# Performance work log

Measured on AMD Instinct MI355X. Metric: run time of the kernel, lower is better.

The kernel has to match this reference:

```python
import jax, jax.numpy as jnp
import numpy as np

NEG_SLOPE = 0.2
EPS = 1e-16


def gat_conv(x, edge_index, W, att_src, att_dst, bias, heads, out_ch, concat):
    """PyG-style GATConv (eval mode, add_self_loops=True)."""
    N = x.shape[0]
    h = (x @ W).reshape(N, heads, out_ch)              # [N,H,C]
    loop = jnp.arange(N, dtype=edge_index.dtype)
    src = jnp.concatenate([edge_index[0], loop])       # [E+N]
    dst = jnp.concatenate([edge_index[1], loop])
    a_src = jnp.sum(h * att_src, axis=-1)              # [N,H]
    a_dst = jnp.sum(h * att_dst, axis=-1)
    e = jax.nn.leaky_relu(a_src[src] + a_dst[dst], NEG_SLOPE)  # [E+N,H]
    # segment softmax over destination nodes
    m = jax.ops.segment_max(e, dst, num_segments=N)
    e = jnp.exp(e - m[dst])
    s = jax.ops.segment_sum(e, dst, num_segments=N)
    alpha = e / (s[dst] + EPS)                         # [E+N,H]
    msg = h[src] * alpha[..., None]                    # [E+N,H,C]
    out = jax.ops.segment_sum(msg, dst, num_segments=N)  # [N,H,C]
    out = out.reshape(N, heads * out_ch) if concat else out.mean(axis=1)
    return out + bias


def setup_inputs() -> dict:
    key = jax.random.key(0)
    ks = jax.random.split(key, 11)
    N, F, E = 100000, 128, 1600000
    H1, C1 = 4, 16
    H2, C2 = 1, 16
    return {
        "x": jax.random.normal(ks[0], (N, F), dtype=jnp.float32),
        "edge_index": jax.random.randint(ks[1], (2, E), 0, N, dtype=jnp.int64) if jax.config.jax_enable_x64 else jax.random.randint(ks[1], (2, E), 0, N).astype(jnp.int32),
        "W1": jax.random.normal(ks[2], (F, H1 * C1), dtype=jnp.float32) * 0.1,
        "att_src1": jax.random.normal(ks[3], (H1, C1), dtype=jnp.float32) * 0.1,
        "att_dst1": jax.random.normal(ks[4], (H1, C1), dtype=jnp.float32) * 0.1,
        "bias1": jax.random.normal(ks[5], (H1 * C1,), dtype=jnp.float32) * 0.1,
        "W2": jax.random.normal(ks[6], (H1 * C1, H2 * C2), dtype=jnp.float32) * 0.1,
        "att_src2": jax.random.normal(ks[7], (H2, C2), dtype=jnp.float32) * 0.1,
        "att_dst2": jax.random.normal(ks[8], (H2, C2), dtype=jnp.float32) * 0.1,
        "bias2": jax.random.normal(ks[9], (C2,), dtype=jnp.float32) * 0.1,
    }


def reference(x, edge_index, W1, att_src1, att_dst1, bias1, W2, att_src2, att_dst2, bias2):
    # dropout is identity in eval mode
    h = gat_conv(x, edge_index, W1, att_src1, att_dst1, bias1, heads=4, out_ch=16, concat=True)
    h = jax.nn.elu(h)
    h = gat_conv(h, edge_index, W2, att_src2, att_dst2, bias2, heads=1, out_ch=16, concat=False)
    return jax.nn.log_softmax(h, axis=1)
```

## Files before the change

### kernel.cpp

```cpp
#include <hip/hip_runtime.h>
#include <hip/hip_fp16.h>
#include <hip/hip_bf16.h>
#include <math.h>


#define LRELU(v) ((v) > 0.f ? (v) : 0.2f * (v))
#define BSH 8
#define BCAP 5120
#define CHK 8192

typedef __attribute__((ext_vector_type(8))) short short8;
typedef __attribute__((ext_vector_type(8))) _Float16 half8;
typedef __attribute__((ext_vector_type(4))) _Float16 half4;
typedef __attribute__((ext_vector_type(4))) float float4v;

static __device__ __forceinline__ short f2bf(float f) {
    __hip_bfloat16 b = __float2bfloat16(f);
    return *reinterpret_cast<short*>(&b);
}

__global__ __launch_bounds__(256) void k_scatter(const int* __restrict__ ei, int* __restrict__ cursor,
                                                 int* __restrict__ stage, int E, int NBK) {
    __shared__ int hist[512];
    __shared__ int cnt2[512];
    __shared__ int base[512];
    int tid = threadIdx.x;
    int e0 = blockIdx.x * CHK;
    int nedge = E - e0; if (nedge > CHK) nedge = CHK;

    for (int i = tid; i < 512; i += 256) { hist[i] = 0; cnt2[i] = 0; }
    __syncthreads();
    for (int j = tid; j < nedge; j += 256) {
        int d = ei[E + e0 + j];
        atomicAdd(&hist[d >> BSH], 1);
    }
    __syncthreads();
    for (int b = tid; b < NBK; b += 256) {
        int c = hist[b];
        if (c > 0) base[b] = b * BCAP + atomicAdd(&cursor[b], c);
    }
    __syncthreads();
    for (int j = tid; j < nedge; j += 256) {
        int s = ei[e0 + j];
        int d = ei[E + e0 + j];
        int b = d >> BSH;
        int r = atomicAdd(&cnt2[b], 1);
        stage[base[b] + r] = s | ((d & ((1 << BSH) - 1)) << 17);
    }
}

__global__ __launch_bounds__(256) void k_build(const int* __restrict__ stage,
                                               const int* __restrict__ cursor,
                                               int* __restrict__ row_start,
                                               int* __restrict__ csr,
                                               const float* __restrict__ W1,
                                               const float* __restrict__ att_src,
                                               const float* __restrict__ att_dst,
                                               float* __restrict__ Wc,
                                               const float* __restrict__ W2,
                                               const float* __restrict__ att_src2,
                                               const float* __restrict__ att_dst2,
                                               float* __restrict__ Wc2,
                                               int NBK, int E, int N) {
    __shared__ int cnt[256];
    __shared__ int lb[256];
    __shared__ int cur[256];
    __shared__ int sA[256];
    int b = blockIdx.x, tid = threadIdx.x;
    int nodes0 = b << BSH;
    int nnodes = N - nodes0; if (nnodes > 256) nnodes = 256;
    int partial = 0;
    for (int i = tid; i < b; i += 256) partial += cursor[i];
    sA[tid] = partial;
    __syncthreads();
    for (int off = 128; off >= 1; off >>= 1) {
        if (tid < off) sA[tid] += sA[tid + off];
        __syncthreads();
    }
    int ebase = sA[0];
    int ecnt = cursor[b];
    __syncthreads();
    if (b == 0) {
        if (tid == 0) row_start[N] = E + N;
        for (int i = tid; i < 16 * 128; i += 256) {
            int col = i >> 7, k = i & 127;
            float v = 0.f;
            if (col < 8) {
                int h = col & 3;
                const float* att = (col < 4) ? att_src : att_dst;
                #pragma unroll
                for (int c = 0; c < 16; c++) v += W1[k * 64 + h * 16 + c] * att[h * 16 + c];
            }
            Wc[i] = v;
        }
        for (int i = tid; i < 128; i += 256) {
            int col = i >> 6, k = i & 63;
            const float* att = col ? att_dst2 : att_src2;
            float v = 0.f;
            #pragma unroll
            for (int c = 0; c < 16; c++) v += W2[k * 16 + c] * att[c];
            Wc2[i] = v;
        }
    }
    const int* sbk = stage + b * BCAP;
    cnt[tid] = (tid < nnodes) ? 1 : 0;
    __syncthreads();
    for (int e = tid; e < ecnt; e += 256) {
        int l = (sbk[e] >> 17) & 255;
        atomicAdd(&cnt[l], 1);
    }
    __syncthreads();
    int myc = cnt[tid];
    sA[tid] = myc;
    __syncthreads();
    for (int off = 1; off < 256; off <<= 1) {
        int r = sA[tid] + ((tid >= off) ? sA[tid - off] : 0);
        __syncthreads();
        sA[tid] = r;
        __syncthreads();
    }
    int gb = ebase + nodes0;
    lb[tid] = sA[tid] - myc;
    cur[tid] = 1;
    __syncthreads();
    if (tid < nnodes) {
        row_start[nodes0 + tid] = gb + lb[tid];
        csr[gb + lb[tid]] = nodes0 + tid;
    }
    __syncthreads();
    for (int e = tid; e < ecnt; e += 256) {
        int v = sbk[e];
        int l = (v >> 17) & 255;
        int src = v & 0x1FFFF;
        int r = atomicAdd(&cur[l], 1);
        csr[gb + lb[l] + r] = src;
    }
}

__global__ __launch_bounds__(256) void k_gemm1(const float* __restrict__ x,
                                               const float* __restrict__ W1,
                                               const float* __restrict__ Wc,
                                               __half* __restrict__ h1, float* __restrict__ a_src,
                                               float* __restrict__ a_dst, int N) {
    __shared__ short wt[80 * 136];
    int tid = threadIdx.x;
    for (int i = tid; i < 128 * 64; i += 256) {
        int k = i >> 6, c = i & 63;
        wt[c * 136 + k] = f2bf(W1[i]);
    }
    for (int i = tid; i < 16 * 128; i += 256) {
        int col = i >> 7, k = i & 127;
        wt[(64 + col) * 136 + k] = f2bf(Wc[i]);
    }
    __syncthreads();
    int wave = tid >> 6, lane = tid & 63;
    int m = lane & 15, q = lane >> 4;
    int nbase = blockIdx.x * 64 + wave * 16;
    int anode = nbase + m;
    bool rowok = anode < N;
    const float* xrow = x + (size_t)(rowok ? anode : 0) * 128 + q * 8;

    float4v acc[5];
    #pragma unroll
    for (int ct = 0; ct < 5; ct++)
        #pragma unroll
        for (int r = 0; r < 4; r++) acc[ct][r] = 0.f;

    #pragma unroll
    for (int kc = 0; kc < 4; kc++) {
        float4 u0 = make_float4(0.f, 0.f, 0.f, 0.f), u1 = u0;
        if (rowok) {
            u0 = *(const float4*)(xrow + kc * 32);
            u1 = *(const float4*)(xrow + kc * 32 + 4);
        }
        short8 af;
        af[0] = f2bf(u0.x); af[1] = f2bf(u0.y); af[2] = f2bf(u0.z); af[3] = f2bf(u0.w);
        af[4] = f2bf(u1.x); af[5] = f2bf(u1.y); af[6] = f2bf(u1.z); af[7] = f2bf(u1.w);
        #pragma unroll
        for (int ct = 0; ct < 5; ct++) {
            short8 bf = *(const short8*)&wt[(ct * 16 + m) * 136 + kc * 32 + q * 8];
            acc[ct] = __builtin_amdgcn_mfma_f32_16x16x32_bf16(af, bf, acc[ct], 0, 0, 0);
        }
    }
    #pragma unroll
    for (int ct = 0; ct < 4; ct++) {
        #pragma unroll
        for (int r = 0; r < 4; r++) {
            int n = nbase + q * 4 + r;
            if (n < N) h1[(size_t)n * 64 + ct * 16 + m] = __float2half(acc[ct][r]);
        }
    }
    #pragma unroll
    for (int r = 0; r < 4; r++) {
        int n = nbase + q * 4 + r;
        if (n < N) {
            float v = acc[4][r];
            if (m < 4) a_src[n * 4 + m] = v;
            else if (m < 8) a_dst[n * 4 + (m - 4)] = v;
        }
    }
}

__global__ __launch_bounds__(256) void k_agg1(const int* __restrict__ row_start,
                                              const int* __restrict__ csr_src,
                                              const float* __restrict__ a_src,
                                              const float* __restrict__ a_dst,
                                              const __half* __restrict__ h1,
                                              const float* __restrict__ bias,
                                              __half* __restrict__ out1, int N) {
    int tid = threadIdx.x;
    int wave = tid >> 6, lane = tid & 63;
    int grp = lane >> 3, sub = lane & 3, par = (lane >> 2) & 1;
    int node = blockIdx.x * 32 + wave * 8 + grp;
    if (node >= N) return;
    int row = row_start[node];
    int deg = row_start[node + 1] - row;
    float adm = a_dst[node * 4 + sub];
    const _Float16* hb = (const _Float16*)h1 + sub * 16;
    const int* cp = csr_src + row + par;
    float A[16];
    #pragma unroll
    for (int c = 0; c < 16; c++) A[c] = 0.f;
    float sh = 0.f;
    int c0 = 0, c1 = 0, c2 = 0, c3 = 0;
    if (deg >= 8) { c0 = cp[0]; c1 = cp[2]; c2 = cp[4]; c3 = cp[6]; }
    int j = 0;
    for (; j + 8 <= deg; j += 8) {
        int s0 = c0, s1 = c1, s2 = c2, s3 = c3;
        float x0 = a_src[s0 * 4 + sub] + adm;
        float x1 = a_src[s1 * 4 + sub] + adm;
        float x2 = a_src[s2 * 4 + sub] + adm;
        float x3 = a_src[s3 * 4 + sub] + adm;
        half8 p0 = *(const half8*)(hb + (size_t)s0 * 64);
        half8 q0 = *(const half8*)(hb + (size_t)s0 * 64 + 8);
        half8 p1 = *(const half8*)(hb + (size_t)s1 * 64);
        half8 q1 = *(const half8*)(hb + (size_t)s1 * 64 + 8);
        half8 p2 = *(const half8*)(hb + (size_t)s2 * 64);
        half8 q2 = *(const half8*)(hb + (size_t)s2 * 64 + 8);
        half8 p3 = *(const half8*)(hb + (size_t)s3 * 64);
        half8 q3 = *(const half8*)(hb + (size_t)s3 * 64 + 8);
        if (j + 16 <= deg) {
            c0 = cp[j + 8]; c1 = cp[j + 10]; c2 = cp[j + 12]; c3 = cp[j + 14];
        }
        float e0 = __expf(fmaxf(x0, 0.2f * x0));
        float e1 = __expf(fmaxf(x1, 0.2f * x1));
        float e2 = __expf(fmaxf(x2, 0.2f * x2));
        float e3 = __expf(fmaxf(x3, 0.2f * x3));
        sh += (e0 + e1) + (e2 + e3);
        #pragma unroll
        for (int c = 0; c < 8; c++) {
            A[c]     += e0 * (float)p0[c] + e1 * (float)p1[c]
                      + e2 * (float)p2[c] + e3 * (float)p3[c];
            A[c + 8] += e0 * (float)q0[c] + e1 * (float)q1[c]
                      + e2 * (float)q2[c] + e3 * (float)q3[c];
        }
    }
    for (; j < deg; j += 2) {
        int idx = j + par;
        if (idx < deg) {
            int s = csr_src[row + idx];
            float xv = a_src[s * 4 + sub] + adm;
            half8 p = *(const half8*)(hb + (size_t)s * 64);
            half8 q = *(const half8*)(hb + (size_t)s * 64 + 8);
            float e = __expf(fmaxf(xv, 0.2f * xv));
            sh += e;
            #pragma unroll
            for (int c = 0; c < 8; c++) {
                A[c]     += e * (float)p[c];
                A[c + 8] += e * (float)q[c];
            }
        }
    }
    sh += __shfl_xor(sh, 4, 64);
    #pragma unroll
    for (int c = 0; c < 16; c++) A[c] += __shfl_xor(A[c], 4, 64);
    if (par == 0) {
        float iv = 1.f / (sh + 1e-16f);
        const float4* bb = (const float4*)bias + sub * 4;
        union { __half2 h2v[8]; float4 f4[2]; } pk;
        #pragma unroll
        for (int c4 = 0; c4 < 4; c4++) {
            float4 b = bb[c4];
            float o0 = A[c4 * 4 + 0] * iv + b.x;
            float o1 = A[c4 * 4 + 1] * iv + b.y;
            float o2 = A[c4 * 4 + 2] * iv + b.z;
            float o3 = A[c4 * 4 + 3] * iv + b.w;
            o0 = (o0 > 0.f) ? o0 : (__expf(o0) - 1.f);
            o1 = (o1 > 0.f) ? o1 : (__expf(o1) - 1.f);
            o2 = (o2 > 0.f) ? o2 : (__expf(o2) - 1.f);
            o3 = (o3 > 0.f) ? o3 : (__expf(o3) - 1.f);
            pk.h2v[c4 * 2 + 0] = __floats2half2_rn(o0, o1);
            pk.h2v[c4 * 2 + 1] = __floats2half2_rn(o2, o3);
        }
        *(float4*)&out1[(size_t)node * 64 + sub * 16]     = pk.f4[0];
        *(float4*)&out1[(size_t)node * 64 + sub * 16 + 8] = pk.f4[1];
    }
}

__global__ __launch_bounds__(256) void k_gemm2(const __half* __restrict__ out1,
                                               const float* __restrict__ W2,
                                               const float* __restrict__ Wc2,
                                               __half* __restrict__ h2, float* __restrict__ a_src,
                                               float* __restrict__ a_dst, int N) {
    __shared__ _Float16 wt2[16][72];
    __shared__ _Float16 wtb[16][72];
    int tid = threadIdx.x;
    for (int i = tid; i < 16 * 64; i += 256) {
        int k = i >> 4, c = i & 15;
        wt2[c][k] = (_Float16)W2[i];
    }
    for (int i = tid; i < 16 * 64; i += 256) {
        int col = i >> 6, k = i & 63;
        wtb[col][k] = (col < 2) ? (_Float16)Wc2[col * 64 + k] : (_Float16)0.f;
    }
    __syncthreads();
    int wave = tid >> 6, lane = tid & 63;
    int m = lane & 15, q = lane >> 4;
    int nbase = blockIdx.x * 64 + wave * 16;
    int anode = nbase + m;
    bool ok = anode < N;
    const __half* arow = out1 + (size_t)(ok ? anode : 0) * 64 + q * 8;

    float4v c1 = {0.f, 0.f, 0.f, 0.f}, c2v = {0.f, 0.f, 0.f, 0.f};
    #pragma unroll
    for (int kc = 0; kc < 2; kc++) {
        half8 af = *(const half8*)(arow + kc * 32);
        half8 b1 = *(const half8*)&wt2[m][kc * 32 + q * 8];
        half8 b2 = *(const half8*)&wtb[m][kc * 32 + q * 8];
        c1  = __builtin_amdgcn_mfma_f32_16x16x32_f16(af, b1, c1, 0, 0, 0);
        c2v = __builtin_amdgcn_mfma_f32_16x16x32_f16(af, b2, c2v, 0, 0, 0);
    }
    #pragma unroll
    for (int r = 0; r < 4; r++) {
        int n = nbase + q * 4 + r;
        if (n < N) {
            h2[(size_t)n * 16 + m] = __float2half(c1[r]);
            if (m == 0) a_src[n] = c2v[r];
            else if (m == 1) a_dst[n] = c2v[r];
        }
    }
}

__global__ __launch_bounds__(256) void k_agg2(const int* __restrict__ row_start,
                                              const int* __restrict__ csr_src,
                                              const float* __restrict__ a_src,
                                              const float* __restrict__ a_dst,
                                              const __half* __restrict__ h2,
                                              const float* __restrict__ bias,
                                              float* __restrict__ out, int N) {
    int tid = threadIdx.x;
    int wave = tid >> 6, lane = tid & 63;
    int grp = lane >> 3, sub = lane & 3, par = (lane >> 2) & 1;
    int node = blockIdx.x * 32 + wave * 8 + grp;
    if (node >= N) return;
    int row = row_start[node];
    int deg = row_start[node + 1] - row;
    float ad = a_dst[node];
    const _Float16* hb = (const _Float16*)h2 + sub * 4;
    const int* cp = csr_src + row + par;
    float A0 = 0.f, A1 = 0.f, A2 = 0.f, A3 = 0.f;
    float sh = 0.f;
    int c0 = 0, c1 = 0, c2 = 0, c3 = 0;
    if (deg >= 8) { c0 = cp[0]; c1 = cp[2]; c2 = cp[4]; c3 = cp[6]; }
    int j = 0;
    for (; j + 8 <= deg; j += 8) {
        int s0 = c0, s1 = c1, s2 = c2, s3 = c3;
        float x0 = a_src[s0] + ad;
        float x1 = a_src[s1] + ad;
        float x2 = a_src[s2] + ad;
        float x3 = a_src[s3] + ad;
        half4 v0 = *(const half4*)(hb + (size_t)s0 * 16);
        half4 v1 = *(const half4*)(hb + (size_t)s1 * 16);
        half4 v2 = *(const half4*)(hb + (size_t)s2 * 16);
        half4 v3 = *(const half4*)(hb + (size_t)s3 * 16);
        if (j + 16 <= deg) {
            c0 = cp[j + 8]; c1 = cp[j + 10]; c2 = cp[j + 12]; c3 = cp[j + 14];
        }
        float e0 = __expf(fmaxf(x0, 0.2f * x0));
        float e1 = __expf(fmaxf(x1, 0.2f * x1));
        float e2 = __expf(fmaxf(x2, 0.2f * x2));
        float e3 = __expf(fmaxf(x3, 0.2f * x3));
        sh += (e0 + e1) + (e2 + e3);
        A0 += e0 * (float)v0[0] + e1 * (float)v1[0] + e2 * (float)v2[0] + e3 * (float)v3[0];
        A1 += e0 * (float)v0[1] + e1 * (float)v1[1] + e2 * (float)v2[1] + e3 * (float)v3[1];
        A2 += e0 * (float)v0[2] + e1 * (float)v1[2] + e2 * (float)v2[2] + e3 * (float)v3[2];
        A3 += e0 * (float)v0[3] + e1 * (float)v1[3] + e2 * (float)v2[3] + e3 * (float)v3[3];
    }
    for (; j < deg; j += 2) {
        int idx = j + par;
        if (idx < deg) {
            int s = csr_src[row + idx];
            float xv = a_src[s] + ad;
            half4 v = *(const half4*)(hb + (size_t)s * 16);
            float e = __expf(fmaxf(xv, 0.2f * xv));
            sh += e;
            A0 += e * (float)v[0];
            A1 += e * (float)v[1];
            A2 += e * (float)v[2];
            A3 += e * (float)v[3];
        }
    }
    sh += __shfl_xor(sh, 4, 64);
    A0 += __shfl_xor(A0, 4, 64);
    A1 += __shfl_xor(A1, 4, 64);
    A2 += __shfl_xor(A2, 4, 64);
    A3 += __shfl_xor(A3, 4, 64);
    float iv = 1.f / (sh + 1e-16f);
    float4 b = ((const float4*)bias)[sub];
    float v0 = A0 * iv + b.x;
    float v1 = A1 * iv + b.y;
    float v2 = A2 * iv + b.z;
    float v3 = A3 * iv + b.w;
    float mx = fmaxf(fmaxf(v0, v1), fmaxf(v2, v3));
    mx = fmaxf(mx, __shfl_xor(mx, 1, 64));
    mx = fmaxf(mx, __shfl_xor(mx, 2, 64));
    float se = __expf(v0 - mx) + __expf(v1 - mx) + __expf(v2 - mx) + __expf(v3 - mx);
    se += __shfl_xor(se, 1, 64);
    se += __shfl_xor(se, 2, 64);
    float ls = mx + __logf(se);
    if (par == 0)
        *(float4*)&out[(size_t)node * 16 + sub * 4] =
            make_float4(v0 - ls, v1 - ls, v2 - ls, v3 - ls);
}

extern "C" void kernel_launch(void* const* d_in, const int* in_sizes, int n_in,
                              void* d_out, int out_size, void* d_ws, size_t ws_size,
                              hipStream_t stream) {
    const float* x        = (const float*)d_in[0];
    const int*   ei       = (const int*)d_in[1];
    const float* W1       = (const float*)d_in[2];
    const float* att_src1 = (const float*)d_in[3];
    const float* att_dst1 = (const float*)d_in[4];
    const float* bias1    = (const float*)d_in[5];
    const float* W2       = (const float*)d_in[6];
    const float* att_src2 = (const float*)d_in[7];
    const float* att_dst2 = (const float*)d_in[8];
    const float* bias2    = (const float*)d_in[9];
    float* out = (float*)d_out;

    const int N = in_sizes[0] / 128;
    const int E = in_sizes[1] / 2;
    const int NBK = (N + 255) >> BSH;

    char* p = (char*)d_ws;
    auto alloc = [&](size_t bytes) -> void* {
        void* r = (void*)p;
        p += (bytes + 255) & ~(size_t)255;
        return r;
    };
    __half* h1     = (__half*)alloc((size_t)N * 64 * 2);
    __half* out1   = (__half*)alloc((size_t)N * 64 * 2);
    __half* h2     = (__half*)alloc((size_t)N * 16 * 2);
    float* a_src1  = (float*)alloc((size_t)N * 4 * 4);
    float* a_dst1  = (float*)alloc((size_t)N * 4 * 4);
    float* a_src2  = (float*)alloc((size_t)N * 4);
    float* a_dst2  = (float*)alloc((size_t)N * 4);
    float* Wc      = (float*)alloc(16 * 128 * 4);
    float* Wc2     = (float*)alloc(2 * 64 * 4);
    int*   row_st  = (int*)alloc((size_t)(N + 1) * 4);
    int*   csr     = (int*)alloc((size_t)(E + N) * 4);
    int*   stage   = (int*)alloc((size_t)NBK * BCAP * 4);
    int*   cursor  = (int*)alloc((size_t)NBK * 4);
    (void)ws_size; (void)n_in; (void)out_size;

    hipMemsetAsync(cursor, 0, (size_t)NBK * 4, stream);
    k_scatter<<<(E + CHK - 1) / CHK, 256, 0, stream>>>(ei, cursor, stage, E, NBK);
    k_build<<<NBK, 256, 0, stream>>>(stage, cursor, row_st, csr,
                                     W1, att_src1, att_dst1, Wc,
                                     W2, att_src2, att_dst2, Wc2, NBK, E, N);
    k_gemm1<<<(N + 63) / 64, 256, 0, stream>>>(x, W1, Wc, h1, a_src1, a_dst1, N);
    k_agg1<<<(N + 31) / 32, 256, 0, stream>>>(row_st, csr, a_src1, a_dst1, h1, bias1, out1, N);
    k_gemm2<<<(N + 63) / 64, 256, 0, stream>>>(out1, W2, Wc2, h2, a_src2, a_dst2, N);
    k_agg2<<<(N + 31) / 32, 256, 0, stream>>>(row_st, csr, a_src2, a_dst2, h2, bias2, out, N);
}
```

Measured before the change: 229.4 us.

## Merge scatter with GEMM1, fuse GEMM2 into agg1, widen agg2 edge parallelism

The edge-scatter and the first GEMM (now folding the attention projection in-kernel) run as disjoint block ranges of a single launch, so they overlap. The second layer's linear transform and attention logits are computed inside the layer-1 aggregation epilogue using a small shared W2, which removes the out1 round-trip and one launch. agg2 now uses 16 lanes per node (4 edge-parallel groups) instead of 8, which adds extra shuffle reductions. Precision changes slightly because GEMM2 now runs in fp32 on CUDA cores instead of fp16 MFMA.

```diff
diff --git a/kernel.cpp b/kernel.cpp
--- a/kernel.cpp
+++ b/kernel.cpp
@@ -19,33 +19,106 @@
     return *reinterpret_cast<short*>(&b);
 }
 
-__global__ __launch_bounds__(256) void k_scatter(const int* __restrict__ ei, int* __restrict__ cursor,
-                                                 int* __restrict__ stage, int E, int NBK) {
-    __shared__ int hist[512];
-    __shared__ int cnt2[512];
-    __shared__ int base[512];
+__global__ __launch_bounds__(256) void k_pre(const int* __restrict__ ei, int* __restrict__ cursor,
+                                             int* __restrict__ stage, int E, int NBK,
+                                             const float* __restrict__ x,
+                                             const float* __restrict__ W1,
+                                             const float* __restrict__ att_src1,
+                                             const float* __restrict__ att_dst1,
+                                             __half* __restrict__ h1,
+                                             float* __restrict__ a_src, float* __restrict__ a_dst,
+                                             int N, int GS) {
+    __shared__ __align__(16) char smem[80 * 136 * 2];
     int tid = threadIdx.x;
-    int e0 = blockIdx.x * CHK;
-    int nedge = E - e0; if (nedge > CHK) nedge = CHK;
-
-    for (int i = tid; i < 512; i += 256) { hist[i] = 0; cnt2[i] = 0; }
-    __syncthreads();
-    for (int j = tid; j < nedge; j += 256) {
-        int d = ei[E + e0 + j];
-        atomicAdd(&hist[d >> BSH], 1);
-    }
-    __syncthreads();
-    for (int b = tid; b < NBK; b += 256) {
-        int c = hist[b];
-        if (c > 0) base[b] = b * BCAP + atomicAdd(&cursor[b], c);
-    }
-    __syncthreads();
-    for (int j = tid; j < nedge; j += 256) {
-        int s = ei[e0 + j];
-        int d = ei[E + e0 + j];
-        int b = d >> BSH;
-        int r = atomicAdd(&cnt2[b], 1);
-        stage[base[b] + r] = s | ((d & ((1 << BSH) - 1)) << 17);
+    if (blockIdx.x < GS) {
+        int* hist = (int*)smem;
+        int* cnt2 = hist + 512;
+        int* base = cnt2 + 512;
+        int e0 = blockIdx.x * CHK;
+        int nedge = E - e0; if (nedge > CHK) nedge = CHK;
+        for (int i = tid; i < 512; i += 256) { hist[i] = 0; cnt2[i] = 0; }
+        __syncthreads();
+        for (int j = tid; j < nedge; j += 256) {
+            int d = ei[E + e0 + j];
+            atomicAdd(&hist[d >> BSH], 1);
+        }
+        __syncthreads();
+        for (int b = tid; b < NBK; b += 256) {
+            int c = hist[b];
+            if (c > 0) base[b] = b * BCAP + atomicAdd(&cursor[b], c);
+        }
+        __syncthreads();
+        for (int j = tid; j < nedge; j += 256) {
+            int s = ei[e0 + j];
+            int d = ei[E + e0 + j];
+            int b = d >> BSH;
+            int r = atomicAdd(&cnt2[b], 1);
+            stage[base[b] + r] = s | ((d & ((1 << BSH) - 1)) << 17);
+        }
+    } else {
+        short* wt = (short*)smem;
+        for (int i = tid; i < 128 * 64; i += 256) {
+            int k = i >> 6, c = i & 63;
+            wt[c * 136 + k] = f2bf(W1[i]);
+        }
+        for (int i = tid; i < 16 * 128; i += 256) {
+            int col = i >> 7, k = i & 127;
+            float v = 0.f;
+            if (col < 8) {
+                int h = col & 3;
+                const float* att = (col < 4) ? att_src1 : att_dst1;
+                #pragma unroll
+                for (int c = 0; c < 16; c++) v += W1[k * 64 + h * 16 + c] * att[h * 16 + c];
+            }
+            wt[(64 + col) * 136 + k] = f2bf(v);
+        }
+        __syncthreads();
+        int wave = tid >> 6, lane = tid & 63;
+        int m = lane & 15, q = lane >> 4;
+        int nbase = (blockIdx.x - GS) * 64 + wave * 16;
+        int anode = nbase + m;
+        bool rowok = anode < N;
+        const float* xrow = x + (size_t)(rowok ? anode : 0) * 128 + q * 8;
+
+        float4v acc[5];
+        #pragma unroll
+        for (int ct = 0; ct < 5; ct++)
+            #pragma unroll
+            for (int r = 0; r < 4; r++) acc[ct][r] = 0.f;
+
+        #pragma unroll
+        for (int kc = 0; kc < 4; kc++) {
+            float4 u0 = make_float4(0.f, 0.f, 0.f, 0.f), u1 = u0;
+            if (rowok) {
+                u0 = *(const float4*)(xrow + kc * 32);
+                u1 = *(const float4*)(xrow + kc * 32 + 4);
+            }
+            short8 af;
+            af[0] = f2bf(u0.x); af[1] = f2bf(u0.y); af[2] = f2bf(u0.z); af[3] = f2bf(u0.w);
+            af[4] = f2bf(u1.x); af[5] = f2bf(u1.y); af[6] = f2bf(u1.z); af[7] = f2bf(u1.w);
+            #pragma unroll
+            for (int ct = 0; ct < 5; ct++) {
+                short8 bf = *(const short8*)&wt[(ct * 16 + m) * 136 + kc * 32 + q * 8];
+                acc[ct] = __builtin_amdgcn_mfma_f32_16x16x32_bf16(af, bf, acc[ct], 0, 0, 0);
+            }
+        }
+        #pragma unroll
+        for (int ct = 0; ct < 4; ct++) {
+            #pragma unroll
+            for (int r = 0; r < 4; r++) {
+                int n = nbase + q * 4 + r;
+                if (n < N) h1[(size_t)n * 64 + ct * 16 + m] = __float2half(acc[ct][r]);
+            }
+        }
+        #pragma unroll
+        for (int r = 0; r < 4; r++) {
+            int n = nbase + q * 4 + r;
+            if (n < N) {
+                float v = acc[4][r];
+                if (m < 4) a_src[n * 4 + m] = v;
+                else if (m < 8) a_dst[n * 4 + (m - 4)] = v;
+            }
+        }
     }
 }
 
@@ -53,14 +126,6 @@
                                                const int* __restrict__ cursor,
                                                int* __restrict__ row_start,
                                                int* __restrict__ csr,
-                                               const float* __restrict__ W1,
-                                               const float* __restrict__ att_src,
-                                               const float* __restrict__ att_dst,
-                                               float* __restrict__ Wc,
-                                               const float* __restrict__ W2,
-                                               const float* __restrict__ att_src2,
-                                               const float* __restrict__ att_dst2,
-                                               float* __restrict__ Wc2,
                                                int NBK, int E, int N) {
     __shared__ int cnt[256];
     __shared__ int lb[256];
@@ -80,28 +145,7 @@
     int ebase = sA[0];
     int ecnt = cursor[b];
     __syncthreads();
-    if (b == 0) {
-        if (tid == 0) row_start[N] = E + N;
-        for (int i = tid; i < 16 * 128; i += 256) {
-            int col = i >> 7, k = i & 127;
-            float v = 0.f;
-            if (col < 8) {
-                int h = col & 3;
-                const float* att = (col < 4) ? att_src : att_dst;
-                #pragma unroll
-                for (int c = 0; c < 16; c++) v += W1[k * 64 + h * 16 + c] * att[h * 16 + c];
-            }
-            Wc[i] = v;
-        }
-        for (int i = tid; i < 128; i += 256) {
-            int col = i >> 6, k = i & 63;
-            const float* att = col ? att_dst2 : att_src2;
-            float v = 0.f;
-            #pragma unroll
-            for (int c = 0; c < 16; c++) v += W2[k * 16 + c] * att[c];
-            Wc2[i] = v;
-        }
-    }
+    if (b == 0 && tid == 0) row_start[N] = E + N;
     const int* sbk = stage + b * BCAP;
     cnt[tid] = (tid < nnodes) ? 1 : 0;
     __syncthreads();
@@ -137,78 +181,24 @@
     }
 }
 
-__global__ __launch_bounds__(256) void k_gemm1(const float* __restrict__ x,
-                                               const float* __restrict__ W1,
-                                               const float* __restrict__ Wc,
-                                               __half* __restrict__ h1, float* __restrict__ a_src,
-                                               float* __restrict__ a_dst, int N) {
-    __shared__ short wt[80 * 136];
+__global__ __launch_bounds__(256) void k_agg1f(const int* __restrict__ row_start,
+                                               const int* __restrict__ csr_src,
+                                               const float* __restrict__ a_src,
+                                               const float* __restrict__ a_dst,
+                                               const __half* __restrict__ h1,
+                                               const float* __restrict__ bias,
+                                               const float* __restrict__ W2,
+                                               const float* __restrict__ att_src2,
+                                               const float* __restrict__ att_dst2,
+                                               __half* __restrict__ h2,
+                                               float* __restrict__ a_src2,
+                                               float* __restrict__ a_dst2, int N) {
+    __shared__ float sW2[64 * 16];
+    __shared__ float sAs[16], sAd[16];
     int tid = threadIdx.x;
-    for (int i = tid; i < 128 * 64; i += 256) {
-        int k = i >> 6, c = i & 63;
-        wt[c * 136 + k] = f2bf(W1[i]);
-    }
-    for (int i = tid; i < 16 * 128; i += 256) {
-        int col = i >> 7, k = i & 127;
-        wt[(64 + col) * 136 + k] = f2bf(Wc[i]);
-    }
-    __syncthreads();
-    int wave = tid >> 6, lane = tid & 63;
-    int m = lane & 15, q = lane >> 4;
-    int nbase = blockIdx.x * 64 + wave * 16;
-    int anode = nbase + m;
-    bool rowok = anode < N;
-    const float* xrow = x + (size_t)(rowok ? anode : 0) * 128 + q * 8;
-
-    float4v acc[5];
-    #pragma unroll
-    for (int ct = 0; ct < 5; ct++)
-        #pragma unroll
-        for (int r = 0; r < 4; r++) acc[ct][r] = 0.f;
-
-    #pragma unroll
-    for (int kc = 0; kc < 4; kc++) {
-        float4 u0 = make_float4(0.f, 0.f, 0.f, 0.f), u1 = u0;
-        if (rowok) {
-            u0 = *(const float4*)(xrow + kc * 32);
-            u1 = *(const float4*)(xrow + kc * 32 + 4);
-        }
-        short8 af;
-        af[0] = f2bf(u0.x); af[1] = f2bf(u0.y); af[2] = f2bf(u0.z); af[3] = f2bf(u0.w);
-        af[4] = f2bf(u1.x); af[5] = f2bf(u1.y); af[6] = f2bf(u1.z); af[7] = f2bf(u1.w);
-        #pragma unroll
-        for (int ct = 0; ct < 5; ct++) {
-            short8 bf = *(const short8*)&wt[(ct * 16 + m) * 136 + kc * 32 + q * 8];
-            acc[ct] = __builtin_amdgcn_mfma_f32_16x16x32_bf16(af, bf, acc[ct], 0, 0, 0);
-        }
-    }
-    #pragma unroll
-    for (int ct = 0; ct < 4; ct++) {
-        #pragma unroll
-        for (int r = 0; r < 4; r++) {
-            int n = nbase + q * 4 + r;
-            if (n < N) h1[(size_t)n * 64 + ct * 16 + m] = __float2half(acc[ct][r]);
-        }
-    }
-    #pragma unroll
-    for (int r = 0; r < 4; r++) {
-        int n = nbase + q * 4 + r;
-        if (n < N) {
-            float v = acc[4][r];
-            if (m < 4) a_src[n * 4 + m] = v;
-            else if (m < 8) a_dst[n * 4 + (m - 4)] = v;
-        }
-    }
-}
-
-__global__ __launch_bounds__(256) void k_agg1(const int* __restrict__ row_start,
-                                              const int* __restrict__ csr_src,
-                                              const float* __restrict__ a_src,
-                                              const float* __restrict__ a_dst,
-                                              const __half* __restrict__ h1,
-                                              const float* __restrict__ bias,
-                                              __half* __restrict__ out1, int N) {
-    int tid = threadIdx.x;
+    for (int i = tid; i < 1024; i += 256) sW2[i] = W2[i];
+    if (tid < 16) { sAs[tid] = att_src2[tid]; sAd[tid] = att_dst2[tid]; }
+    __syncthreads();
     int wave = tid >> 6, lane = tid & 63;
     int grp = lane >> 3, sub = lane & 3, par = (lane >> 2) & 1;
     int node = blockIdx.x * 32 + wave * 8 + grp;
@@ -274,71 +264,53 @@
     sh += __shfl_xor(sh, 4, 64);
     #pragma unroll
     for (int c = 0; c < 16; c++) A[c] += __shfl_xor(A[c], 4, 64);
-    if (par == 0) {
-        float iv = 1.f / (sh + 1e-16f);
-        const float4* bb = (const float4*)bias + sub * 4;
-        union { __half2 h2v[8]; float4 f4[2]; } pk;
-        #pragma unroll
-        for (int c4 = 0; c4 < 4; c4++) {
-            float4 b = bb[c4];
-            float o0 = A[c4 * 4 + 0] * iv + b.x;
-            float o1 = A[c4 * 4 + 1] * iv + b.y;
-            float o2 = A[c4 * 4 + 2] * iv + b.z;
-            float o3 = A[c4 * 4 + 3] * iv + b.w;
-            o0 = (o0 > 0.f) ? o0 : (__expf(o0) - 1.f);
-            o1 = (o1 > 0.f) ? o1 : (__expf(o1) - 1.f);
-            o2 = (o2 > 0.f) ? o2 : (__expf(o2) - 1.f);
-            o3 = (o3 > 0.f) ? o3 : (__expf(o3) - 1.f);
-            pk.h2v[c4 * 2 + 0] = __floats2half2_rn(o0, o1);
-            pk.h2v[c4 * 2 + 1] = __floats2half2_rn(o2, o3);
-        }
-        *(float4*)&out1[(size_t)node * 64 + sub * 16]     = pk.f4[0];
-        *(float4*)&out1[(size_t)node * 64 + sub * 16 + 8] = pk.f4[1];
-    }
-}
-
-__global__ __launch_bounds__(256) void k_gemm2(const __half* __restrict__ out1,
-                                               const float* __restrict__ W2,
-                                               const float* __restrict__ Wc2,
-                                               __half* __restrict__ h2, float* __restrict__ a_src,
-                                               float* __restrict__ a_dst, int N) {
-    __shared__ _Float16 wt2[16][72];
-    __shared__ _Float16 wtb[16][72];
-    int tid = threadIdx.x;
-    for (int i = tid; i < 16 * 64; i += 256) {
-        int k = i >> 4, c = i & 15;
-        wt2[c][k] = (_Float16)W2[i];
-    }
-    for (int i = tid; i < 16 * 64; i += 256) {
-        int col = i >> 6, k = i & 63;
-        wtb[col][k] = (col < 2) ? (_Float16)Wc2[col * 64 + k] : (_Float16)0.f;
-    }
-    __syncthreads();
-    int wave = tid >> 6, lane = tid & 63;
-    int m = lane & 15, q = lane >> 4;
-    int nbase = blockIdx.x * 64 + wave * 16;
-    int anode = nbase + m;
-    bool ok = anode < N;
-    const __half* arow = out1 + (size_t)(ok ? anode : 0) * 64 + q * 8;
-
-    float4v c1 = {0.f, 0.f, 0.f, 0.f}, c2v = {0.f, 0.f, 0.f, 0.f};
-    #pragma unroll
-    for (int kc = 0; kc < 2; kc++) {
-        half8 af = *(const half8*)(arow + kc * 32);
-        half8 b1 = *(const half8*)&wt2[m][kc * 32 + q * 8];
-        half8 b2 = *(const half8*)&wtb[m][kc * 32 + q * 8];
-        c1  = __builtin_amdgcn_mfma_f32_16x16x32_f16(af, b1, c1, 0, 0, 0);
-        c2v = __builtin_amdgcn_mfma_f32_16x16x32_f16(af, b2, c2v, 0, 0, 0);
-    }
-    #pragma unroll
-    for (int r = 0; r < 4; r++) {
-        int n = nbase + q * 4 + r;
-        if (n < N) {
-            h2[(size_t)n * 16 + m] = __float2half(c1[r]);
-            if (m == 0) a_src[n] = c2v[r];
-            else if (m == 1) a_dst[n] = c2v[r];
-        }
-    }
+    float iv = 1.f / (sh + 1e-16f);
+    const float4* bb = (const float4*)bias + sub * 4;
+    float o[16];
+    #pragma unroll
+    for (int c4 = 0; c4 < 4; c4++) {
+        float4 b = bb[c4];
+        float o0 = A[c4 * 4 + 0] * iv + b.x;
+        float o1 = A[c4 * 4 + 1] * iv + b.y;
+        float o2 = A[c4 * 4 + 2] * iv + b.z;
+        float o3 = A[c4 * 4 + 3] * iv + b.w;
+        o[c4 * 4 + 0] = (o0 > 0.f) ? o0 : (__expf(o0) - 1.f);
+        o[c4 * 4 + 1] = (o1 > 0.f) ? o1 : (__expf(o1) - 1.f);
+        o[c4 * 4 + 2] = (o2 > 0.f) ? o2 : (__expf(o2) - 1.f);
+        o[c4 * 4 + 3] = (o3 > 0.f) ? o3 : (__expf(o3) - 1.f);
+    }
+    float pk[8];
+    #pragma unroll
+    for (int kk = 0; kk < 8; kk++) pk[kk] = 0.f;
+    #pragma unroll
+    for (int cc = 0; cc < 16; cc++) {
+        float ov = o[cc];
+        const float* wr = &sW2[(sub * 16 + cc) * 16 + par * 8];
+        #pragma unroll
+        for (int kk = 0; kk < 8; kk++) pk[kk] += ov * wr[kk];
+    }
+    #pragma unroll
+    for (int kk = 0; kk < 8; kk++) {
+        pk[kk] += __shfl_xor(pk[kk], 1, 64);
+        pk[kk] += __shfl_xor(pk[kk], 2, 64);
+    }
+    if (sub == 0) {
+        union { __half2 hh[4]; float4 f; } u;
+        u.hh[0] = __floats2half2_rn(pk[0], pk[1]);
+        u.hh[1] = __floats2half2_rn(pk[2], pk[3]);
+        u.hh[2] = __floats2half2_rn(pk[4], pk[5]);
+        u.hh[3] = __floats2half2_rn(pk[6], pk[7]);
+        *(float4*)&h2[(size_t)node * 16 + par * 8] = u.f;
+    }
+    float ps = 0.f, pd = 0.f;
+    #pragma unroll
+    for (int kk = 0; kk < 8; kk++) {
+        ps += pk[kk] * sAs[par * 8 + kk];
+        pd += pk[kk] * sAd[par * 8 + kk];
+    }
+    ps += __shfl_xor(ps, 4, 64);
+    pd += __shfl_xor(pd, 4, 64);
+    if (sub == 0 && par == 0) { a_src2[node] = ps; a_dst2[node] = pd; }
 }
 
 __global__ __launch_bounds__(256) void k_agg2(const int* __restrict__ row_start,
@@ -350,8 +322,8 @@
                                               float* __restrict__ out, int N) {
     int tid = threadIdx.x;
     int wave = tid >> 6, lane = tid & 63;
-    int grp = lane >> 3, sub = lane & 3, par = (lane >> 2) & 1;
-    int node = blockIdx.x * 32 + wave * 8 + grp;
+    int grp = lane >> 4, sub = lane & 3, par = (lane >> 2) & 3;
+    int node = blockIdx.x * 16 + wave * 4 + grp;
     if (node >= N) return;
     int row = row_start[node];
     int deg = row_start[node + 1] - row;
@@ -361,9 +333,9 @@
     float A0 = 0.f, A1 = 0.f, A2 = 0.f, A3 = 0.f;
     float sh = 0.f;
     int c0 = 0, c1 = 0, c2 = 0, c3 = 0;
-    if (deg >= 8) { c0 = cp[0]; c1 = cp[2]; c2 = cp[4]; c3 = cp[6]; }
+    if (deg >= 16) { c0 = cp[0]; c1 = cp[4]; c2 = cp[8]; c3 = cp[12]; }
     int j = 0;
-    for (; j + 8 <= deg; j += 8) {
+    for (; j + 16 <= deg; j += 16) {
         int s0 = c0, s1 = c1, s2 = c2, s3 = c3;
         float x0 = a_src[s0] + ad;
         float x1 = a_src[s1] + ad;
@@ -373,8 +345,8 @@
         half4 v1 = *(const half4*)(hb + (size_t)s1 * 16);
         half4 v2 = *(const half4*)(hb + (size_t)s2 * 16);
         half4 v3 = *(const half4*)(hb + (size_t)s3 * 16);
-        if (j + 16 <= deg) {
-            c0 = cp[j + 8]; c1 = cp[j + 10]; c2 = cp[j + 12]; c3 = cp[j + 14];
+        if (j + 32 <= deg) {
+            c0 = cp[j + 16]; c1 = cp[j + 20]; c2 = cp[j + 24]; c3 = cp[j + 28];
         }
         float e0 = __expf(fmaxf(x0, 0.2f * x0));
         float e1 = __expf(fmaxf(x1, 0.2f * x1));
@@ -386,7 +358,7 @@
         A2 += e0 * (float)v0[2] + e1 * (float)v1[2] + e2 * (float)v2[2] + e3 * (float)v3[2];
         A3 += e0 * (float)v0[3] + e1 * (float)v1[3] + e2 * (float)v2[3] + e3 * (float)v3[3];
     }
-    for (; j < deg; j += 2) {
+    for (; j < deg; j += 4) {
         int idx = j + par;
         if (idx < deg) {
             int s = csr_src[row + idx];
@@ -400,11 +372,11 @@
             A3 += e * (float)v[3];
         }
     }
-    sh += __shfl_xor(sh, 4, 64);
-    A0 += __shfl_xor(A0, 4, 64);
-    A1 += __shfl_xor(A1, 4, 64);
-    A2 += __shfl_xor(A2, 4, 64);
-    A3 += __shfl_xor(A3, 4, 64);
+    sh += __shfl_xor(sh, 4, 64);  sh += __shfl_xor(sh, 8, 64);
+    A0 += __shfl_xor(A0, 4, 64);  A0 += __shfl_xor(A0, 8, 64);
+    A1 += __shfl_xor(A1, 4, 64);  A1 += __shfl_xor(A1, 8, 64);
+    A2 += __shfl_xor(A2, 4, 64);  A2 += __shfl_xor(A2, 8, 64);
+    A3 += __shfl_xor(A3, 4, 64);  A3 += __shfl_xor(A3, 8, 64);
     float iv = 1.f / (sh + 1e-16f);
     float4 b = ((const float4*)bias)[sub];
     float v0 = A0 * iv + b.x;
@@ -441,6 +413,8 @@
     const int N = in_sizes[0] / 128;
     const int E = in_sizes[1] / 2;
     const int NBK = (N + 255) >> BSH;
+    const int GS = (E + CHK - 1) / CHK;
+    const int GG = (N + 63) / 64;
 
     char* p = (char*)d_ws;
     auto alloc = [&](size_t bytes) -> void* {
@@ -449,14 +423,11 @@
         return r;
     };
     __half* h1     = (__half*)alloc((size_t)N * 64 * 2);
-    __half* out1   = (__half*)alloc((size_t)N * 64 * 2);
     __half* h2     = (__half*)alloc((size_t)N * 16 * 2);
     float* a_src1  = (float*)alloc((size_t)N * 4 * 4);
     float* a_dst1  = (float*)alloc((size_t)N * 4 * 4);
     float* a_src2  = (float*)alloc((size_t)N * 4);
     float* a_dst2  = (float*)alloc((size_t)N * 4);
-    float* Wc      = (float*)alloc(16 * 128 * 4);
-    float* Wc2     = (float*)alloc(2 * 64 * 4);
     int*   row_st  = (int*)alloc((size_t)(N + 1) * 4);
     int*   csr     = (int*)alloc((size_t)(E + N) * 4);
     int*   stage   = (int*)alloc((size_t)NBK * BCAP * 4);
@@ -464,12 +435,12 @@
     (void)ws_size; (void)n_in; (void)out_size;
 
     hipMemsetAsync(cursor, 0, (size_t)NBK * 4, stream);
-    k_scatter<<<(E + CHK - 1) / CHK, 256, 0, stream>>>(ei, cursor, stage, E, NBK);
-    k_build<<<NBK, 256, 0, stream>>>(stage, cursor, row_st, csr,
-                                     W1, att_src1, att_dst1, Wc,
-                                     W2, att_src2, att_dst2, Wc2, NBK, E, N);
-    k_gemm1<<<(N + 63) / 64, 256, 0, stream>>>(x, W1, Wc, h1, a_src1, a_dst1, N);
-    k_agg1<<<(N + 31) / 32, 256, 0, stream>>>(row_st, csr, a_src1, a_dst1, h1, bias1, out1, N);
-    k_gemm2<<<(N + 63) / 64, 256, 0, stream>>>(out1, W2, Wc2, h2, a_src2, a_dst2, N);
-    k_agg2<<<(N + 31) / 32, 256, 0, stream>>>(row_st, csr, a_src2, a_dst2, h2, bias2, out, N);
-}
+    k_pre<<<GS + GG, 256, 0, stream>>>(ei, cursor, stage, E, NBK,
+                                       x, W1, att_src1, att_dst1,
+                                       h1, a_src1, a_dst1, N, GS);
+    k_build<<<NBK, 256, 0, stream>>>(stage, cursor, row_st, csr, NBK, E, N);
+    k_agg1f<<<(N + 31) / 32, 256, 0, stream>>>(row_st, csr, a_src1, a_dst1, h1, bias1,
+                                               W2, att_src2, att_dst2,
+                                               h2, a_src2, a_dst2, N);
+    k_agg2<<<(N + 15) / 16, 256, 0, stream>>>(row_st, csr, a_src2, a_dst2, h2, bias2, out, N);
+}
```

Measured after the change: 229.9 us. No clear change (+0.2%).
